# Optimization experiments

Measured on AMD Instinct MI355X. Metric: run time of the kernel, lower is better.

## Reference

```python
import jax, jax.numpy as jnp
import numpy as np

T, N, F = 4096, 32, 512  # time, batch, num_features (= d_state)
SCALE = 0.02


def setup_inputs() -> dict:
    key = jax.random.key(0)
    ku, ka, kb, kc, kd = jax.random.split(key, 5)
    return {
        "u": jax.random.normal(ku, (T, N, F), dtype=jnp.float32),
        "A": jax.random.normal(ka, (F, F), dtype=jnp.float32) * SCALE,
        "B": jax.random.normal(kb, (F, F), dtype=jnp.float32) * SCALE,
        "C": jax.random.normal(kc, (F, F), dtype=jnp.float32) * SCALE,
        "D": jax.random.normal(kd, (F, F), dtype=jnp.float32) * SCALE,
    }


def reference(u, A, B, C, D):
    # Elman-style tanh SSM: x_t = tanh(x_{t-1} A^T + u_t B^T); y_t = x_t C^T + u_t D^T
    n, d_state = u.shape[1], A.shape[0]

    def step(x, u_t):
        x = jnp.tanh(x @ A.T + u_t @ B.T)      # (N, d_state)
        y_t = x @ C.T + u_t @ D.T              # (N, num_features)
        return x, y_t

    x0 = jnp.zeros((n, d_state), dtype=u.dtype)
    _, ys = jax.lax.scan(step, x0, u)          # ys: (T, N, num_features)
    return ys
```

## Files before the change

kernel.cpp:

```cpp
#include <hip/hip_runtime.h>


typedef unsigned int u32;
typedef __attribute__((ext_vector_type(8))) short short8;
typedef __attribute__((ext_vector_type(4))) short short4v;
typedef __attribute__((ext_vector_type(4))) float f32x4;

#define AS1 __attribute__((address_space(1)))
#define AS3 __attribute__((address_space(3)))

static constexpr int TT     = 4096;
static constexpr int NBATCH = 32;
static constexpr int FD     = 512;
static constexpr int M_TOT  = TT * NBATCH;
static constexpr int CHUNK  = 32;
static constexpr int WARM   = 32;
static constexpr int NCHUNK = TT / CHUNK;
static constexpr int NGRP   = NCHUNK * 2;
static constexpr int KREG   = 384;
static constexpr int TN     = FD * NBATCH;
static constexpr int NWGG   = (M_TOT / 256) * (FD / 128);

static constexpr int XROW = 1040;
static constexpr int AROW = 272;
static constexpr int TROW = 528;
static constexpr int GBUF = 24576;
static constexpr int BOFF = 16384;

#define BAR() asm volatile("s_waitcnt lgkmcnt(0)\n\ts_barrier" ::: "memory")

__device__ __forceinline__ unsigned short f2bf(float f) {
  u32 u = __builtin_bit_cast(u32, f);
  u32 r = u + 0x7FFFu + ((u >> 16) & 1u);
  return (unsigned short)(r >> 16);
}
__device__ __forceinline__ unsigned short f2bf_fast(float f) {
  u32 u = __builtin_bit_cast(u32, f);
  return (unsigned short)((u + 0x8000u) >> 16);
}
__device__ __forceinline__ float bf2f(unsigned short h) {
  u32 u = ((u32)h) << 16;
  return __builtin_bit_cast(float, u);
}
__device__ __forceinline__ u32 pack_bf2(float a, float b) {
  __bf16 x = (__bf16)a, y = (__bf16)b;
  return (u32)__builtin_bit_cast(unsigned short, x) |
         ((u32)__builtin_bit_cast(unsigned short, y) << 16);
}

typedef __attribute__((ext_vector_type(8))) __bf16 bf16x8;
__device__ __forceinline__ f32x4 mfma16(short8 a, short8 b, f32x4 c) {
  return __builtin_amdgcn_mfma_f32_16x16x32_bf16(
      __builtin_bit_cast(bf16x8, a), __builtin_bit_cast(bf16x8, b), c, 0, 0, 0);
}

__global__ void cvt_k(const float* __restrict__ A, const float* __restrict__ B,
                      const float* __restrict__ C, const float* __restrict__ D,
                      unsigned short* __restrict__ Ab, unsigned short* __restrict__ Bb,
                      unsigned short* __restrict__ Cb, unsigned short* __restrict__ Db) {
  const float* s;
  unsigned short* d;
  switch (blockIdx.y) {
    case 0: s = A; d = Ab; break;
    case 1: s = B; d = Bb; break;
    case 2: s = C; d = Cb; break;
    default: s = D; d = Db; break;
  }
  int i = (blockIdx.x * blockDim.x + threadIdx.x) * 4;
  float4 f = *(const float4*)(s + i);
  short4v v;
  v[0] = (short)f2bf(f.x); v[1] = (short)f2bf(f.y);
  v[2] = (short)f2bf(f.z); v[3] = (short)f2bf(f.w);
  *(short4v*)(d + i) = v;
}

__global__ __launch_bounds__(256) void cvt_u_k(const float* __restrict__ u,
                                               unsigned short* __restrict__ ubf) {
  const int stride = gridDim.x * blockDim.x;
  const int total = M_TOT * (FD / 4);
  for (int idx = blockIdx.x * blockDim.x + threadIdx.x; idx < total; idx += stride) {
    float4 f = *(const float4*)(u + (size_t)idx * 4);
    short4v v;
    v[0] = (short)f2bf(f.x); v[1] = (short)f2bf(f.y);
    v[2] = (short)f2bf(f.z); v[3] = (short)f2bf(f.w);
    *(short4v*)(ubf + (size_t)idx * 4) = v;
  }
}


__device__ __forceinline__ void stage_a_bf16(const unsigned short* __restrict__ src,
                                             int row0, int k0, char* buf,
                                             int w, int l) {
  const int rsub = l >> 2;
  const int csw = ((l & 3) ^ (rsub & 3)) * 8;
  #pragma unroll
  for (int j = 0; j < 2; ++j) {
    const int q = w * 2 + j;
    const unsigned short* gp =
        src + (size_t)(row0 + q * 16 + rsub) * FD + k0 + csw;
    __builtin_amdgcn_global_load_lds((const AS1 u32*)gp,
                                     (AS3 u32*)(buf + q * 1024), 16, 0, 0);
  }
}
__device__ __forceinline__ void stage_b_bf16(const unsigned short* __restrict__ src,
                                             int row0, int k0, char* buf,
                                             int w, int l) {
  const int rsub = l >> 2;
  const int csw = ((l & 3) ^ (rsub & 3)) * 8;
  const unsigned short* gp =
      src + (size_t)(row0 + w * 16 + rsub) * FD + k0 + csw;
  __builtin_amdgcn_global_load_lds((const AS1 u32*)gp,
                                   (AS3 u32*)(buf + BOFF + w * 1024), 16, 0, 0);
}

__device__ __forceinline__ void compute32(const char* buf, f32x4 (&acc)[4][4],
                                          int wr, int wc, int lr, int g) {
  const int co = (g ^ (lr & 3)) * 16;
  short8 af[4], bf[4];
  #pragma unroll
  for (int mi = 0; mi < 4; ++mi)
    af[mi] = *(const short8*)(buf + (wr * 64 + mi * 16 + lr) * 64 + co);
  #pragma unroll
  for (int ni = 0; ni < 4; ++ni)
    bf[ni] = *(const short8*)(buf + BOFF + (wc * 64 + ni * 16 + lr) * 64 + co);
  __builtin_amdgcn_s_setprio(1);
  #pragma unroll
  for (int mi = 0; mi < 4; ++mi)
    #pragma unroll
    for (int ni = 0; ni < 4; ++ni)
      acc[mi][ni] = mfma16(af[mi], bf[ni], acc[mi][ni]);
  __builtin_amdgcn_s_setprio(0);
}

__device__ __forceinline__ void swzgrid(int bid, int& m0, int& i0) {
  int wg = (bid & 7) * (NWGG >> 3) + (bid >> 3);
  m0 = (wg >> 2) * 256;
  i0 = (wg & 3) * 128;
}

__global__ __launch_bounds__(512, 4) void gemm_ub_k(const unsigned short* __restrict__ ubf,
                                                    const unsigned short* __restrict__ Bb,
                                                    unsigned short* __restrict__ ubT) {
  __shared__ __align__(16) char smem[67584];
  const int tid = threadIdx.x, l = tid & 63, w = tid >> 6;
  const int wr = w >> 1, wc = w & 1, lr = l & 15, g = l >> 4;
  int m0, i0;
  swzgrid(blockIdx.x, m0, i0);
  f32x4 acc[4][4];
  #pragma unroll
  for (int mi = 0; mi < 4; ++mi)
    #pragma unroll
    for (int ni = 0; ni < 4; ++ni) acc[mi][ni] = (f32x4){0.f, 0.f, 0.f, 0.f};
  stage_a_bf16(ubf, m0, 0, smem, w, l);
  stage_b_bf16(Bb, i0, 0, smem, w, l);
  __syncthreads();
  for (int kt = 0; kt < 16; ++kt) {
    char* bufC = smem + (kt & 1) * GBUF;
    char* bufN = smem + ((kt + 1) & 1) * GBUF;
    if (kt < 15) {
      stage_a_bf16(ubf, m0, (kt + 1) * 32, bufN, w, l);
      stage_b_bf16(Bb, i0, (kt + 1) * 32, bufN, w, l);
    }
    compute32(bufC, acc, wr, wc, lr, g);
    __syncthreads();
  }
  #pragma unroll
  for (int mi = 0; mi < 4; ++mi)
    #pragma unroll
    for (int ni = 0; ni < 4; ++ni) {
      const int mb = wr * 64 + mi * 16 + g * 4;
      const int il = wc * 64 + ni * 16 + lr;
      uint2 v;
      v.x = pack_bf2(acc[mi][ni][0], acc[mi][ni][1]);
      v.y = pack_bf2(acc[mi][ni][2], acc[mi][ni][3]);
      *(uint2*)(smem + il * TROW + mb * 2) = v;
    }
  __syncthreads();
  const int iG = tid >> 2, sub = tid & 3, t0 = m0 >> 5;
  #pragma unroll
  for (int tl = 0; tl < 8; ++tl) {
    short8 v = *(const short8*)(smem + iG * TROW + (tl * 32 + sub * 8) * 2);
    *(short8*)(ubT + (size_t)(t0 + tl) * TN + (size_t)(i0 + iG) * NBATCH + sub * 8) = v;
  }
}

__global__ __launch_bounds__(512, 4) void gemm_y_k(const unsigned short* __restrict__ xh,
                                                   const unsigned short* __restrict__ ubf,
                                                   const unsigned short* __restrict__ Cb,
                                                   const unsigned short* __restrict__ Db,
                                                   float* __restrict__ y) {
  __shared__ __align__(16) char smem[2 * GBUF];
  const int tid = threadIdx.x, l = tid & 63, w = tid >> 6;
  const int wr = w >> 1, wc = w & 1, lr = l & 15, g = l >> 4;
  int m0, i0;
  swzgrid(blockIdx.x, m0, i0);
  f32x4 acc[4][4];
  #pragma unroll
  for (int mi = 0; mi < 4; ++mi)
    #pragma unroll
    for (int ni = 0; ni < 4; ++ni) acc[mi][ni] = (f32x4){0.f, 0.f, 0.f, 0.f};
  stage_a_bf16(xh, m0, 0, smem, w, l);
  stage_b_bf16(Cb, i0, 0, smem, w, l);
  __syncthreads();
  for (int kt = 0; kt < 32; ++kt) {
    char* bufC = smem + (kt & 1) * GBUF;
    char* bufN = smem + ((kt + 1) & 1) * GBUF;
    if (kt < 31) {
      const int nxt = kt + 1;
      const unsigned short* asrc = (nxt < 16) ? xh : ubf;
      const unsigned short* bsrc = (nxt < 16) ? Cb : Db;
      const int k0 = (nxt & 15) * 32;
      stage_a_bf16(asrc, m0, k0, bufN, w, l);
      stage_b_bf16(bsrc, i0, k0, bufN, w, l);
    }
    compute32(bufC, acc, wr, wc, lr, g);
    __syncthreads();
  }
  #pragma unroll
  for (int mi = 0; mi < 4; ++mi)
    #pragma unroll
    for (int ni = 0; ni < 4; ++ni) {
      const int ig = i0 + wc * 64 + ni * 16 + lr;
      const size_t mb = (size_t)(m0 + wr * 64 + mi * 16 + g * 4);
      #pragma unroll
      for (int r = 0; r < 4; ++r)
        y[(mb + r) * FD + ig] = acc[mi][ni][r];
    }
}

__global__ __launch_bounds__(512) void serial_k(const unsigned short* __restrict__ Ab,
                                                const unsigned short* __restrict__ ubT,
                                                unsigned short* __restrict__ xhist) {
  __shared__ __align__(16) unsigned char AldsB[512 * AROW];
  __shared__ __align__(16) unsigned char xbufB[16 * XROW];
  const int tid = threadIdx.x;
  const int l = tid & 63, w = tid >> 6;
  const int lr = l & 15, g = l >> 4;
  const int b = blockIdx.x;
  const int chunk = b >> 1, nh = b & 1, n0 = nh * 16;
  const int tstart = chunk * CHUNK;
  const int t0 = (chunk == 0) ? 0 : tstart - WARM;
  const int nsteps = tstart + CHUNK - t0;

  short8 areg[4][12];
  #pragma unroll
  for (int ct = 0; ct < 4; ++ct) {
    const int i = w * 64 + ct * 16 + lr;
    #pragma unroll
    for (int kb = 0; kb < 12; ++kb)
      areg[ct][kb] = *(const short8*)(Ab + (size_t)i * FD + kb * 32 + g * 8);
  }
  for (int rr = 0; rr < 16; ++rr) {
    const int row = rr * 32 + (tid >> 4);
    const int kc = tid & 15;
    short8 v = *(const short8*)(Ab + (size_t)row * FD + KREG + kc * 8);
    *(short8*)(AldsB + row * AROW + kc * 16) = v;
  }
  BAR();

  const unsigned short* ubp =
      ubT + (size_t)t0 * TN + (size_t)(w * 64 + lr) * NBATCH + n0 + g * 4;
  unsigned short* xhp =
      xhist + ((size_t)t0 * NBATCH + n0 + g * 4) * FD + w * 64 + lr;
  const unsigned char* xread = xbufB + lr * XROW + g * 16;
  unsigned char* xwrite = xbufB + (g * 4) * XROW + (w * 64 + lr) * 2;
  const unsigned char* aldsr[4];
  #pragma unroll
  for (int ct = 0; ct < 4; ++ct)
    aldsr[ct] = AldsB + (w * 64 + ct * 16 + lr) * AROW + g * 16;

  short4v ubr[4];
  #pragma unroll
  for (int ct = 0; ct < 4; ++ct) ubr[ct] = *(const short4v*)(ubp + ct * 512);
  ubp += TN;

  for (int s = 0; s < nsteps; ++s) {
    const int t = t0 + s;
    f32x4 acc[4];
    #pragma unroll
    for (int ct = 0; ct < 4; ++ct)
      #pragma unroll
      for (int r = 0; r < 4; ++r) acc[ct][r] = bf2f((unsigned short)ubr[ct][r]);
    if (s + 1 < nsteps) {
      #pragma unroll
      for (int ct = 0; ct < 4; ++ct) ubr[ct] = *(const short4v*)(ubp + ct * 512);
    }
    ubp += TN;
    if (s > 0) {
      #pragma unroll
      for (int kb = 0; kb < 12; ++kb) {
        short8 xf = *(const short8*)(xread + kb * 64);
        #pragma unroll
        for (int ct = 0; ct < 4; ++ct) acc[ct] = mfma16(xf, areg[ct][kb], acc[ct]);
      }
      #pragma unroll
      for (int kb2 = 0; kb2 < 4; ++kb2) {
        short8 xf = *(const short8*)(xread + (12 + kb2) * 64);
        #pragma unroll
        for (int ct = 0; ct < 4; ++ct) {
          short8 af = *(const short8*)(aldsr[ct] + kb2 * 64);
          acc[ct] = mfma16(xf, af, acc[ct]);
        }
      }
    }
    unsigned short hv[4][4];
    #pragma unroll
    for (int ct = 0; ct < 4; ++ct)
      #pragma unroll
      for (int r = 0; r < 4; ++r) {
        float e = __expf(2.f * acc[ct][r]);
        hv[ct][r] = f2bf_fast(1.f - 2.f * __builtin_amdgcn_rcpf(e + 1.f));
      }
    if (t >= tstart) {
      #pragma unroll
      for (int ct = 0; ct < 4; ++ct)
        #pragma unroll
        for (int r = 0; r < 4; ++r) xhp[r * FD + ct * 16] = hv[ct][r];
    }
    xhp += (size_t)NBATCH * FD;
    BAR();
    #pragma unroll
    for (int ct = 0; ct < 4; ++ct)
      #pragma unroll
      for (int r = 0; r < 4; ++r)
        *(unsigned short*)(xwrite + r * XROW + ct * 32) = hv[ct][r];
    BAR();
  }
}

extern "C" void kernel_launch(void* const* d_in, const int* in_sizes, int n_in,
                              void* d_out, int out_size, void* d_ws, size_t ws_size,
                              hipStream_t stream) {
  const float* u = (const float*)d_in[0];
  const float* A = (const float*)d_in[1];
  const float* B = (const float*)d_in[2];
  const float* C = (const float*)d_in[3];
  const float* D = (const float*)d_in[4];
  float* y = (float*)d_out;

  char* ws = (char*)d_ws;
  size_t off = 0;
  unsigned short* ubT = (unsigned short*)(ws + off);   off += (size_t)M_TOT * FD * 2;
  unsigned short* xhist = (unsigned short*)(ws + off); off += (size_t)M_TOT * FD * 2;
  unsigned short* Ab = (unsigned short*)(ws + off);    off += (size_t)FD * FD * 2;
  unsigned short* Bb = (unsigned short*)(ws + off);    off += (size_t)FD * FD * 2;
  unsigned short* Cb = (unsigned short*)(ws + off);    off += (size_t)FD * FD * 2;
  unsigned short* Db = (unsigned short*)(ws + off);    off += (size_t)FD * FD * 2;
  unsigned short* ubf = (unsigned short*)(ws + off);   off += (size_t)M_TOT * FD * 2;

  cvt_k<<<dim3(FD * FD / (256 * 4), 4), 256, 0, stream>>>(A, B, C, D, Ab, Bb, Cb, Db);
  cvt_u_k<<<dim3(2048, 1), 256, 0, stream>>>(u, ubf);
  gemm_ub_k<<<dim3(NWGG, 1), 512, 0, stream>>>(ubf, Bb, ubT);
  serial_k<<<dim3(NGRP, 1), 512, 0, stream>>>(Ab, ubT, xhist);
  gemm_y_k<<<dim3(NWGG, 1), 512, 0, stream>>>(xhist, ubf, Cb, Db, y);
}
```

Baseline: 531.0 us.

## Triple-buffer GEMM LDS staging with prefetch distance two and vmcnt-based barriers

Both bulk GEMM kernels (u·B^T projection and y output) now use three LDS buffers with loads issued two K-steps ahead. A single barrier per iteration waits on vmcnt instead of a full __syncthreads. This lets global loads overlap more compute and removes one barrier per step. It raises LDS use to 72KB per block, which may lower occupancy, and it depends on stage functions issuing exactly the expected number of direct-to-LDS loads for vmcnt(3) to be correct.

```diff
diff --git a/kernel.cpp b/kernel.cpp
--- a/kernel.cpp
+++ b/kernel.cpp
@@ -28,6 +28,9 @@
 static constexpr int BOFF = 16384;
 
 #define BAR() asm volatile("s_waitcnt lgkmcnt(0)\n\ts_barrier" ::: "memory")
+#define GBAR(N) do { \
+    asm volatile("s_waitcnt vmcnt(" #N ") lgkmcnt(0)\n\ts_barrier" ::: "memory"); \
+    __builtin_amdgcn_sched_barrier(0); } while (0)
 
 __device__ __forceinline__ unsigned short f2bf(float f) {
   u32 u = __builtin_bit_cast(u32, f);
@@ -141,7 +144,7 @@
 __global__ __launch_bounds__(512, 4) void gemm_ub_k(const unsigned short* __restrict__ ubf,
                                                     const unsigned short* __restrict__ Bb,
                                                     unsigned short* __restrict__ ubT) {
-  __shared__ __align__(16) char smem[67584];
+  __shared__ __align__(16) char smem[73728];
   const int tid = threadIdx.x, l = tid & 63, w = tid >> 6;
   const int wr = w >> 1, wc = w & 1, lr = l & 15, g = l >> 4;
   int m0, i0;
@@ -153,17 +156,20 @@
     for (int ni = 0; ni < 4; ++ni) acc[mi][ni] = (f32x4){0.f, 0.f, 0.f, 0.f};
   stage_a_bf16(ubf, m0, 0, smem, w, l);
   stage_b_bf16(Bb, i0, 0, smem, w, l);
+  stage_a_bf16(ubf, m0, 32, smem + GBUF, w, l);
+  stage_b_bf16(Bb, i0, 32, smem + GBUF, w, l);
+  int bi = 0;
+  for (int kt = 0; kt < 16; ++kt) {
+    if (kt < 15) { GBAR(3); } else { GBAR(0); }
+    compute32(smem + bi * GBUF, acc, wr, wc, lr, g);
+    if (kt + 2 < 16) {
+      int bn = bi + 2; if (bn >= 3) bn -= 3;
+      stage_a_bf16(ubf, m0, (kt + 2) * 32, smem + bn * GBUF, w, l);
+      stage_b_bf16(Bb, i0, (kt + 2) * 32, smem + bn * GBUF, w, l);
+    }
+    if (++bi == 3) bi = 0;
+  }
   __syncthreads();
-  for (int kt = 0; kt < 16; ++kt) {
-    char* bufC = smem + (kt & 1) * GBUF;
-    char* bufN = smem + ((kt + 1) & 1) * GBUF;
-    if (kt < 15) {
-      stage_a_bf16(ubf, m0, (kt + 1) * 32, bufN, w, l);
-      stage_b_bf16(Bb, i0, (kt + 1) * 32, bufN, w, l);
-    }
-    compute32(bufC, acc, wr, wc, lr, g);
-    __syncthreads();
-  }
   #pragma unroll
   for (int mi = 0; mi < 4; ++mi)
     #pragma unroll
@@ -189,7 +195,7 @@
                                                    const unsigned short* __restrict__ Cb,
                                                    const unsigned short* __restrict__ Db,
                                                    float* __restrict__ y) {
-  __shared__ __align__(16) char smem[2 * GBUF];
+  __shared__ __align__(16) char smem[73728];
   const int tid = threadIdx.x, l = tid & 63, w = tid >> 6;
   const int wr = w >> 1, wc = w & 1, lr = l & 15, g = l >> 4;
   int m0, i0;
@@ -201,20 +207,22 @@
     for (int ni = 0; ni < 4; ++ni) acc[mi][ni] = (f32x4){0.f, 0.f, 0.f, 0.f};
   stage_a_bf16(xh, m0, 0, smem, w, l);
   stage_b_bf16(Cb, i0, 0, smem, w, l);
-  __syncthreads();
+  stage_a_bf16(xh, m0, 32, smem + GBUF, w, l);
+  stage_b_bf16(Cb, i0, 32, smem + GBUF, w, l);
+  int bi = 0;
   for (int kt = 0; kt < 32; ++kt) {
-    char* bufC = smem + (kt & 1) * GBUF;
-    char* bufN = smem + ((kt + 1) & 1) * GBUF;
-    if (kt < 31) {
-      const int nxt = kt + 1;
-      const unsigned short* asrc = (nxt < 16) ? xh : ubf;
-      const unsigned short* bsrc = (nxt < 16) ? Cb : Db;
-      const int k0 = (nxt & 15) * 32;
-      stage_a_bf16(asrc, m0, k0, bufN, w, l);
-      stage_b_bf16(bsrc, i0, k0, bufN, w, l);
-    }
-    compute32(bufC, acc, wr, wc, lr, g);
-    __syncthreads();
+    if (kt < 31) { GBAR(3); } else { GBAR(0); }
+    compute32(smem + bi * GBUF, acc, wr, wc, lr, g);
+    if (kt + 2 < 32) {
+      const int s = kt + 2;
+      const unsigned short* asrc = (s < 16) ? xh : ubf;
+      const unsigned short* bsrc = (s < 16) ? Cb : Db;
+      const int k0 = (s & 15) * 32;
+      int bn = bi + 2; if (bn >= 3) bn -= 3;
+      stage_a_bf16(asrc, m0, k0, smem + bn * GBUF, w, l);
+      stage_b_bf16(bsrc, i0, k0, smem + bn * GBUF, w, l);
+    }
+    if (++bi == 3) bi = 0;
   }
   #pragma unroll
   for (int mi = 0; mi < 4; ++mi)
```

Result: no change. 520.8 us (-1.9%).
